# Kernel optimization log

Measured on AMD Instinct MI355X. Metric: run time of the kernel, lower is better.

## Reference

```python
import jax, jax.numpy as jnp
import numpy as np
import math

H = 16
D_MODEL = 1024
D_K = D_MODEL // H
MAX_REL = 32
B, S = 2, 2048


def setup_inputs() -> dict:
    key = jax.random.key(0)
    ks = jax.random.split(key, 12)
    def w(k):
        return jax.random.normal(k, (D_MODEL, D_MODEL), jnp.float32) * 0.02
    def b(k):
        return jax.random.normal(k, (D_MODEL,), jnp.float32) * 0.02
    return {
        "query": jax.random.normal(ks[0], (B, S, D_MODEL), jnp.float32),
        "key": jax.random.normal(ks[1], (B, S, D_MODEL), jnp.float32),
        "value": jax.random.normal(ks[2], (B, S, D_MODEL), jnp.float32),
        "mask": jax.random.randint(ks[3], (B, S, S), 0, 2, jnp.int32),
        "Wq": w(ks[4]), "bq": b(ks[5]),
        "Wk": w(ks[6]), "bk": b(ks[7]),
        "Wv": w(ks[8]), "bv": b(ks[9]),
        "Wo": w(ks[10]), "bo": b(ks[11]),
        "rel_emb": jax.random.normal(jax.random.fold_in(key, 99), (2 * MAX_REL + 1, D_K), jnp.float32) * 0.02,
    }


def _rel_bias(q_len, k_len, rel_emb):
    # relative positions clamped to [-MAX_REL, MAX_REL], shifted to [0, 2*MAX_REL]
    rel = jnp.arange(q_len)[:, None] - jnp.arange(k_len)[None, :]
    rel = jnp.clip(rel, -MAX_REL, MAX_REL) + MAX_REL
    # embedding lookup then sum over d_k (torch code: permute(2,0,1).sum(0))
    return rel_emb[rel].sum(-1)  # [q_len, k_len], shared across heads/batch


def reference(query, key, value, mask, Wq, bq, Wk, bk, Wv, bv, Wo, bo, rel_emb):
    nb, qlen, _ = query.shape
    klen = key.shape[1]
    def proj(x, W, b):  # torch Linear: x @ W.T + b -> [B, L, H, D_K] -> [B, H, L, D_K]
        return (x @ W.T + b).reshape(nb, -1, H, D_K).transpose(0, 2, 1, 3)
    q = proj(query, Wq, bq)
    k = proj(key, Wk, bk)
    v = proj(value, Wv, bv)
    scores = jnp.einsum('bhqd,bhkd->bhqk', q, k) / math.sqrt(D_K)
    scores = scores + _rel_bias(qlen, klen, rel_emb)[None, None]
    scores = jnp.where(mask[:, None] == 0, -1e9, scores)
    p = jax.nn.softmax(scores, axis=-1)
    out = jnp.einsum('bhqk,bhkd->bhqd', p, v)
    out = out.transpose(0, 2, 1, 3).reshape(nb, -1, H * D_K)
    return out @ Wo.T + bo
```

## Files before the change

### kernel.cpp

```cpp
#include <hip/hip_runtime.h>
#include <hip/hip_bf16.h>
#include <stdint.h>
#include <math.h>

typedef __bf16 bf16;
typedef __attribute__((ext_vector_type(8))) __bf16 bf16x8;
typedef __attribute__((ext_vector_type(4))) float f32x4;

#define MFMA(a, b, c) __builtin_amdgcn_mfma_f32_16x16x32_bf16(a, b, c, 0, 0, 0)

__device__ __forceinline__ bf16x8 cvt8(const float* p) {
  f32x4 a = *(const f32x4*)p;
  f32x4 b = *(const f32x4*)(p + 4);
  bf16x8 o;
  o[0] = (bf16)a[0]; o[1] = (bf16)a[1]; o[2] = (bf16)a[2]; o[3] = (bf16)a[3];
  o[4] = (bf16)b[0]; o[5] = (bf16)b[1]; o[6] = (bf16)b[2]; o[7] = (bf16)b[3];
  return o;
}

__global__ __launch_bounds__(256) void cvt_bf16(
    const float* __restrict__ s0, const float* __restrict__ s1, const float* __restrict__ s2,
    const float* __restrict__ s3, const float* __restrict__ s4, const float* __restrict__ s5,
    const float* __restrict__ s6,
    bf16* __restrict__ d0, bf16* __restrict__ d1, bf16* __restrict__ d2,
    bf16* __restrict__ d3, bf16* __restrict__ d4, bf16* __restrict__ d5,
    bf16* __restrict__ d6) {
  const float* s; bf16* d; int n8;
  switch (blockIdx.y) {
    case 0: s = s0; d = d0; n8 = 524288; break;
    case 1: s = s1; d = d1; n8 = 524288; break;
    case 2: s = s2; d = d2; n8 = 524288; break;
    case 3: s = s3; d = d3; n8 = 131072; break;
    case 4: s = s4; d = d4; n8 = 131072; break;
    case 5: s = s5; d = d5; n8 = 131072; break;
    default: s = s6; d = d6; n8 = 131072; break;
  }
  for (int i = blockIdx.x * 256 + threadIdx.x; i < n8; i += gridDim.x * 256)
    *(bf16x8*)&d[(size_t)i * 8] = cvt8(&s[(size_t)i * 8]);
}

__global__ __launch_bounds__(256) void pack_mask(const int* __restrict__ mask,
                                                 unsigned long long* __restrict__ pm,
                                                 int nwords) {
  const int lane = threadIdx.x & 63;
  const int wave = blockIdx.x * (blockDim.x >> 6) + (threadIdx.x >> 6);
  const int nwaves = gridDim.x * (blockDim.x >> 6);
  for (int w = wave; w < nwords; w += nwaves) {
    int m = mask[(size_t)w * 64 + lane];
    unsigned long long bits = __ballot(m != 0);
    if (lane == 0) pm[w] = bits;
  }
}

template <int OUT>
__global__ __launch_bounds__(256) void gemm_bt(const bf16* __restrict__ X,
                                               const bf16* __restrict__ W,
                                               const float* __restrict__ bias,
                                               void* __restrict__ out_) {
  __shared__ __align__(16) bf16 As[128 * 32];
  __shared__ __align__(16) bf16 Bs[64 * 32];
  const int tid = threadIdx.x, lane = tid & 63, w = tid >> 6;
  const int r16 = lane & 15, g4 = lane >> 4;
  const int m0 = blockIdx.x * 128, n0 = blockIdx.y * 64;

  f32x4 acc[4][2] = {};

  const int ra = tid >> 2;
  const int ca = (tid & 3) << 3;

  bf16x8 xa0 = *(const bf16x8*)&X[(size_t)(m0 + ra) * 1024 + ca];
  bf16x8 xa1 = *(const bf16x8*)&X[(size_t)(m0 + 64 + ra) * 1024 + ca];
  bf16x8 xb0 = *(const bf16x8*)&W[(size_t)(n0 + ra) * 1024 + ca];
  *(bf16x8*)&As[ra * 32 + ca] = xa0;
  *(bf16x8*)&As[(ra + 64) * 32 + ca] = xa1;
  *(bf16x8*)&Bs[ra * 32 + ca] = xb0;
  __syncthreads();

  const int wm = (w >> 1) << 6, wn = (w & 1) << 5;

  for (int k0 = 0; k0 < 1024; k0 += 32) {
    if (k0 + 32 < 1024) {
      xa0 = *(const bf16x8*)&X[(size_t)(m0 + ra) * 1024 + k0 + 32 + ca];
      xa1 = *(const bf16x8*)&X[(size_t)(m0 + 64 + ra) * 1024 + k0 + 32 + ca];
      xb0 = *(const bf16x8*)&W[(size_t)(n0 + ra) * 1024 + k0 + 32 + ca];
    }
    bf16x8 af[4], bfr[2];
#pragma unroll
    for (int i = 0; i < 4; i++)
      af[i] = *(const bf16x8*)&As[(wm + i * 16 + r16) * 32 + g4 * 8];
#pragma unroll
    for (int j = 0; j < 2; j++)
      bfr[j] = *(const bf16x8*)&Bs[(wn + j * 16 + r16) * 32 + g4 * 8];
#pragma unroll
    for (int i = 0; i < 4; i++)
#pragma unroll
      for (int j = 0; j < 2; j++)
        acc[i][j] = MFMA(af[i], bfr[j], acc[i][j]);
    __syncthreads();
    if (k0 + 32 < 1024) {
      *(bf16x8*)&As[ra * 32 + ca] = xa0;
      *(bf16x8*)&As[(ra + 64) * 32 + ca] = xa1;
      *(bf16x8*)&Bs[ra * 32 + ca] = xb0;
      __syncthreads();
    }
  }

#pragma unroll
  for (int j = 0; j < 2; j++) {
    const int col = n0 + wn + j * 16 + r16;
    const float bv = bias[col];
#pragma unroll
    for (int i = 0; i < 4; i++) {
      const int row0 = m0 + wm + i * 16 + g4 * 4;
#pragma unroll
      for (int r = 0; r < 4; r++) {
        float v = acc[i][j][r] + bv;
        const int row = row0 + r;
        if (OUT) {
          const int bb = row >> 11, s = row & 2047, h = col >> 6, d = col & 63;
          ((bf16*)out_)[((((size_t)bb * 16 + h) * 2048 + s) << 6) + d] = (bf16)v;
        } else {
          ((float*)out_)[(size_t)row * 1024 + col] = v;
        }
      }
    }
  }
}

__global__ __launch_bounds__(256) void attn_fwd(const bf16* __restrict__ Q,
                                                const bf16* __restrict__ Kb,
                                                const bf16* __restrict__ Vb,
                                                const unsigned long long* __restrict__ pm,
                                                const float* __restrict__ rel,
                                                bf16* __restrict__ ao) {
  constexpr int PAD = 72;
  __shared__ __align__(16) bf16 Ks[64 * PAD];
  __shared__ __align__(16) bf16 Vs[64 * 64];
  __shared__ __align__(16) bf16 Ps[64 * PAD];
  __shared__ float rb[65];

  const int tid = threadIdx.x, lane = tid & 63, w = tid >> 6;
  const int r16 = lane & 15, g4 = lane >> 4;
  const int qt = blockIdx.x;
  const int bh = blockIdx.y;
  const int b = bh >> 4, h = bh & 15;

  const bf16* Qh = Q + (size_t)bh * 2048 * 64;
  const bf16* Kh = Kb + (size_t)bh * 2048 * 64;
  const bf16* Vh = Vb + (size_t)bh * 2048 * 64;

  if (tid < 65) {
    const float* e = rel + tid * 64;
    float s = 0.f;
#pragma unroll
    for (int i = 0; i < 64; i++) s += e[i];
    rb[tid] = s;
  }

  bf16x8 aq[2];
  {
    const int qrow = (qt << 6) + (w << 4) + r16;
    aq[0] = *(const bf16x8*)&Qh[(size_t)qrow * 64 + g4 * 8];
    aq[1] = *(const bf16x8*)&Qh[(size_t)qrow * 64 + 32 + g4 * 8];
  }

  f32x4 acc_o[4] = {};
  float mreg[4] = {-1e30f, -1e30f, -1e30f, -1e30f};
  float lreg[4] = {0.f, 0.f, 0.f, 0.f};

  int skey[2], sf8[2], svcol[2];
#pragma unroll
  for (int cc = 0; cc < 2; cc++) {
    const int c = tid + (cc << 8);
    skey[cc] = c >> 3;
    sf8[cc] = (c & 7) << 3;
    svcol[cc] = (((skey[cc] >> 3) ^ (c & 7)) << 3) | (skey[cc] & 7);
  }

  bf16x8 kreg[2], vreg[2];
#pragma unroll
  for (int cc = 0; cc < 2; cc++) {
    kreg[cc] = *(const bf16x8*)&Kh[(size_t)skey[cc] * 64 + sf8[cc]];
    vreg[cc] = *(const bf16x8*)&Vh[(size_t)skey[cc] * 64 + sf8[cc]];
  }
#pragma unroll
  for (int cc = 0; cc < 2; cc++) {
    *(bf16x8*)&Ks[skey[cc] * PAD + sf8[cc]] = kreg[cc];
#pragma unroll
    for (int j = 0; j < 8; j++) Vs[((sf8[cc] + j) << 6) | svcol[cc]] = vreg[cc][j];
  }
  __syncthreads();

  for (int t = 0; t < 32; t++) {
    if (t < 31) {
#pragma unroll
      for (int cc = 0; cc < 2; cc++) {
        kreg[cc] = *(const bf16x8*)&Kh[(size_t)(((t + 1) << 6) + skey[cc]) * 64 + sf8[cc]];
        vreg[cc] = *(const bf16x8*)&Vh[(size_t)(((t + 1) << 6) + skey[cc]) * 64 + sf8[cc]];
      }
    }
    unsigned long long mw[4];
    const int qrow0 = (qt << 6) + (w << 4) + (g4 << 2);
#pragma unroll
    for (int r = 0; r < 4; r++)
      mw[r] = pm[(size_t)((b << 11) + qrow0 + r) * 32 + t];

    f32x4 sc[4];
#pragma unroll
    for (int f = 0; f < 4; f++) {
      f32x4 a = {};
#pragma unroll
      for (int kk = 0; kk < 2; kk++) {
        bf16x8 bk_ = *(const bf16x8*)&Ks[(f * 16 + r16) * PAD + kk * 32 + g4 * 8];
        a = MFMA(aq[kk], bk_, a);
      }
      sc[f] = a;
    }

    float s_[4][4];
#pragma unroll
    for (int f = 0; f < 4; f++) {
      const int kcol = (t << 6) + (f << 4) + r16;
#pragma unroll
      for (int r = 0; r < 4; r++) {
        int dd = (qrow0 + r) - kcol;
        dd = dd < -32 ? -32 : (dd > 32 ? 32 : dd);
        const bool on = (mw[r] >> ((f << 4) + r16)) & 1ull;
        s_[f][r] = on ? sc[f][r] * 0.125f + rb[dd + 32] : -1e9f;
      }
    }

    float rs[4];
#pragma unroll
    for (int r = 0; r < 4; r++) {
      float v = fmaxf(fmaxf(s_[0][r], s_[1][r]), fmaxf(s_[2][r], s_[3][r]));
#pragma unroll
      for (int d = 1; d < 16; d <<= 1) v = fmaxf(v, __shfl_xor(v, d, 16));
      const float mn = fmaxf(mreg[r], v);
      rs[r] = __expf(mreg[r] - mn);
      mreg[r] = mn;
    }
    float ps_[4] = {0.f, 0.f, 0.f, 0.f};
#pragma unroll
    for (int f = 0; f < 4; f++)
#pragma unroll
      for (int r = 0; r < 4; r++) {
        const float p = __expf(s_[f][r] - mreg[r]);
        ps_[r] += p;
        Ps[(w * 16 + g4 * 4 + r) * PAD + f * 16 + r16] = (bf16)p;
      }
#pragma unroll
    for (int r = 0; r < 4; r++) {
      float v = ps_[r];
#pragma unroll
      for (int d = 1; d < 16; d <<= 1) v += __shfl_xor(v, d, 16);
      lreg[r] = lreg[r] * rs[r] + v;
    }
#pragma unroll
    for (int f = 0; f < 4; f++)
#pragma unroll
      for (int r = 0; r < 4; r++) acc_o[f][r] *= rs[r];

#pragma unroll
    for (int kk = 0; kk < 2; kk++) {
      bf16x8 ap = *(const bf16x8*)&Ps[(w * 16 + r16) * PAD + kk * 32 + g4 * 8];
#pragma unroll
      for (int f = 0; f < 4; f++) {
        const int d = f * 16 + r16;
        bf16x8 bv_ = *(const bf16x8*)&Vs[(d << 6) | ((((kk << 2) + g4) ^ (d >> 3)) << 3)];
        acc_o[f] = MFMA(ap, bv_, acc_o[f]);
      }
    }
    __syncthreads();
    if (t < 31) {
#pragma unroll
      for (int cc = 0; cc < 2; cc++) {
        *(bf16x8*)&Ks[skey[cc] * PAD + sf8[cc]] = kreg[cc];
#pragma unroll
        for (int j = 0; j < 8; j++) Vs[((sf8[cc] + j) << 6) | svcol[cc]] = vreg[cc][j];
      }
      __syncthreads();
    }
  }

  const int qrow0 = (qt << 6) + (w << 4) + (g4 << 2);
#pragma unroll
  for (int r = 0; r < 4; r++) {
    const float inv = 1.f / lreg[r];
#pragma unroll
    for (int f = 0; f < 4; f++) {
      float v = acc_o[f][r] * inv;
      ao[(size_t)((b << 11) + qrow0 + r) * 1024 + (h << 6) + f * 16 + r16] = (bf16)v;
    }
  }
}

extern "C" void kernel_launch(void* const* d_in, const int* in_sizes, int n_in,
                              void* d_out, int out_size, void* d_ws, size_t ws_size,
                              hipStream_t stream) {
  const float* query = (const float*)d_in[0];
  const float* key   = (const float*)d_in[1];
  const float* value = (const float*)d_in[2];
  const int*   mask  = (const int*)d_in[3];
  const float* Wq = (const float*)d_in[4];
  const float* bq = (const float*)d_in[5];
  const float* Wk = (const float*)d_in[6];
  const float* bk = (const float*)d_in[7];
  const float* Wv = (const float*)d_in[8];
  const float* bv = (const float*)d_in[9];
  const float* Wo = (const float*)d_in[10];
  const float* bo = (const float*)d_in[11];
  const float* rel = (const float*)d_in[12];

  char* ws = (char*)d_ws;
  bf16* Qb = (bf16*)ws;
  bf16* Kb = (bf16*)(ws + 8388608);
  bf16* Vb = (bf16*)(ws + 16777216);
  bf16* AO = (bf16*)(ws + 25165824);
  unsigned long long* PM = (unsigned long long*)(ws + 33554432);
  bf16* qc  = (bf16*)(ws + 34603008);
  bf16* kc  = (bf16*)(ws + 42991616);
  bf16* vc  = (bf16*)(ws + 51380224);
  bf16* wqc = (bf16*)(ws + 59768832);
  bf16* wkc = (bf16*)(ws + 61865984);
  bf16* wvc = (bf16*)(ws + 63963136);
  bf16* woc = (bf16*)(ws + 66060288);

  cvt_bf16<<<dim3(256, 7), 256, 0, stream>>>(query, key, value, Wq, Wk, Wv, Wo,
                                             qc, kc, vc, wqc, wkc, wvc, woc);
  pack_mask<<<256, 256, 0, stream>>>(mask, PM, 2 * 2048 * 32);

  dim3 g(32, 16);
  gemm_bt<1><<<g, 256, 0, stream>>>(qc, wqc, bq, Qb);
  gemm_bt<1><<<g, 256, 0, stream>>>(kc, wkc, bk, Kb);
  gemm_bt<1><<<g, 256, 0, stream>>>(vc, wvc, bv, Vb);

  attn_fwd<<<dim3(32, 32), 256, 0, stream>>>(Qb, Kb, Vb, PM, rel, AO);

  gemm_bt<0><<<g, 256, 0, stream>>>(AO, woc, bo, (float*)d_out);
}
```

Baseline: 458.3 us.

## Enlarge GEMM tiles with direct global-to-LDS loads; exp2 softmax and swizzled P tile

The projection GEMM tile grows from 128x64 to 128x128 per block, and operands are loaded straight into LDS with global_load_lds instead of being staged through registers. The register prefetch that used to overlap the next tile's load with compute is gone, so every k-step now waits on a barrier after the load. In attention, log2(e) is folded into the score scale and relative bias so that exp2f replaces __expf. The padded P buffer becomes an XOR-swizzled 64x64 layout to avoid LDS bank conflicts and save shared memory.

```diff
diff --git a/kernel.cpp b/kernel.cpp
--- a/kernel.cpp
+++ b/kernel.cpp
@@ -8,6 +8,13 @@
 typedef __attribute__((ext_vector_type(4))) float f32x4;
 
 #define MFMA(a, b, c) __builtin_amdgcn_mfma_f32_16x16x32_bf16(a, b, c, 0, 0, 0)
+
+typedef __attribute__((address_space(3))) uint32_t lds_u32;
+typedef __attribute__((address_space(1))) const uint32_t glb_u32;
+
+__device__ __forceinline__ void gload16(const void* g, void* l) {
+  __builtin_amdgcn_global_load_lds((glb_u32*)g, (lds_u32*)l, 16, 0, 0);
+}
 
 __device__ __forceinline__ bf16x8 cvt8(const float* p) {
   f32x4 a = *(const f32x4*)p;
@@ -58,55 +65,40 @@
                                                const float* __restrict__ bias,
                                                void* __restrict__ out_) {
   __shared__ __align__(16) bf16 As[128 * 32];
-  __shared__ __align__(16) bf16 Bs[64 * 32];
+  __shared__ __align__(16) bf16 Bs[128 * 32];
   const int tid = threadIdx.x, lane = tid & 63, w = tid >> 6;
   const int r16 = lane & 15, g4 = lane >> 4;
-  const int m0 = blockIdx.x * 128, n0 = blockIdx.y * 64;
-
-  f32x4 acc[4][2] = {};
-
+  const int m0 = blockIdx.x * 128, n0 = blockIdx.y * 128;
+
+  f32x4 acc[4][4] = {};
   const int ra = tid >> 2;
   const int ca = (tid & 3) << 3;
-
-  bf16x8 xa0 = *(const bf16x8*)&X[(size_t)(m0 + ra) * 1024 + ca];
-  bf16x8 xa1 = *(const bf16x8*)&X[(size_t)(m0 + 64 + ra) * 1024 + ca];
-  bf16x8 xb0 = *(const bf16x8*)&W[(size_t)(n0 + ra) * 1024 + ca];
-  *(bf16x8*)&As[ra * 32 + ca] = xa0;
-  *(bf16x8*)&As[(ra + 64) * 32 + ca] = xa1;
-  *(bf16x8*)&Bs[ra * 32 + ca] = xb0;
-  __syncthreads();
-
-  const int wm = (w >> 1) << 6, wn = (w & 1) << 5;
+  const int wm = (w >> 1) << 6, wn = (w & 1) << 6;
 
   for (int k0 = 0; k0 < 1024; k0 += 32) {
-    if (k0 + 32 < 1024) {
-      xa0 = *(const bf16x8*)&X[(size_t)(m0 + ra) * 1024 + k0 + 32 + ca];
-      xa1 = *(const bf16x8*)&X[(size_t)(m0 + 64 + ra) * 1024 + k0 + 32 + ca];
-      xb0 = *(const bf16x8*)&W[(size_t)(n0 + ra) * 1024 + k0 + 32 + ca];
-    }
-    bf16x8 af[4], bfr[2];
+    gload16(&X[(size_t)(m0 + ra) * 1024 + k0 + ca],      &As[w << 9]);
+    gload16(&X[(size_t)(m0 + 64 + ra) * 1024 + k0 + ca], &As[2048 + (w << 9)]);
+    gload16(&W[(size_t)(n0 + ra) * 1024 + k0 + ca],      &Bs[w << 9]);
+    gload16(&W[(size_t)(n0 + 64 + ra) * 1024 + k0 + ca], &Bs[2048 + (w << 9)]);
+    __syncthreads();
+
+    bf16x8 af[4], bfr[4];
 #pragma unroll
     for (int i = 0; i < 4; i++)
       af[i] = *(const bf16x8*)&As[(wm + i * 16 + r16) * 32 + g4 * 8];
 #pragma unroll
-    for (int j = 0; j < 2; j++)
+    for (int j = 0; j < 4; j++)
       bfr[j] = *(const bf16x8*)&Bs[(wn + j * 16 + r16) * 32 + g4 * 8];
 #pragma unroll
     for (int i = 0; i < 4; i++)
 #pragma unroll
-      for (int j = 0; j < 2; j++)
+      for (int j = 0; j < 4; j++)
         acc[i][j] = MFMA(af[i], bfr[j], acc[i][j]);
     __syncthreads();
-    if (k0 + 32 < 1024) {
-      *(bf16x8*)&As[ra * 32 + ca] = xa0;
-      *(bf16x8*)&As[(ra + 64) * 32 + ca] = xa1;
-      *(bf16x8*)&Bs[ra * 32 + ca] = xb0;
-      __syncthreads();
-    }
-  }
-
-#pragma unroll
-  for (int j = 0; j < 2; j++) {
+  }
+
+#pragma unroll
+  for (int j = 0; j < 4; j++) {
     const int col = n0 + wn + j * 16 + r16;
     const float bv = bias[col];
 #pragma unroll
@@ -134,9 +126,10 @@
                                                 const float* __restrict__ rel,
                                                 bf16* __restrict__ ao) {
   constexpr int PAD = 72;
+  constexpr float SCL = 0.125f * 1.44269504f;
   __shared__ __align__(16) bf16 Ks[64 * PAD];
   __shared__ __align__(16) bf16 Vs[64 * 64];
-  __shared__ __align__(16) bf16 Ps[64 * PAD];
+  __shared__ __align__(16) bf16 Ps[64 * 64];
   __shared__ float rb[65];
 
   const int tid = threadIdx.x, lane = tid & 63, w = tid >> 6;
@@ -154,7 +147,7 @@
     float s = 0.f;
 #pragma unroll
     for (int i = 0; i < 64; i++) s += e[i];
-    rb[tid] = s;
+    rb[tid] = s * 1.44269504f;
   }
 
   bf16x8 aq[2];
@@ -226,7 +219,7 @@
         int dd = (qrow0 + r) - kcol;
         dd = dd < -32 ? -32 : (dd > 32 ? 32 : dd);
         const bool on = (mw[r] >> ((f << 4) + r16)) & 1ull;
-        s_[f][r] = on ? sc[f][r] * 0.125f + rb[dd + 32] : -1e9f;
+        s_[f][r] = on ? sc[f][r] * SCL + rb[dd + 32] : -1e9f;
       }
     }
 
@@ -237,17 +230,21 @@
 #pragma unroll
       for (int d = 1; d < 16; d <<= 1) v = fmaxf(v, __shfl_xor(v, d, 16));
       const float mn = fmaxf(mreg[r], v);
-      rs[r] = __expf(mreg[r] - mn);
+      rs[r] = exp2f(mreg[r] - mn);
       mreg[r] = mn;
     }
     float ps_[4] = {0.f, 0.f, 0.f, 0.f};
+    const int qsw = (g4 * 2) & 7;
 #pragma unroll
     for (int f = 0; f < 4; f++)
 #pragma unroll
       for (int r = 0; r < 4; r++) {
-        const float p = __expf(s_[f][r] - mreg[r]);
+        const float p = exp2f(s_[f][r] - mreg[r]);
         ps_[r] += p;
-        Ps[(w * 16 + g4 * 4 + r) * PAD + f * 16 + r16] = (bf16)p;
+        const int qr = (w << 4) + (g4 << 2) + r;
+        const int g = (f << 1) | (r16 >> 3);
+        const int gs = g ^ ((qsw + (r >> 1)) & 7);
+        Ps[(qr << 6) | (gs << 3) | (r16 & 7)] = (bf16)p;
       }
 #pragma unroll
     for (int r = 0; r < 4; r++) {
@@ -263,7 +260,8 @@
 
 #pragma unroll
     for (int kk = 0; kk < 2; kk++) {
-      bf16x8 ap = *(const bf16x8*)&Ps[(w * 16 + r16) * PAD + kk * 32 + g4 * 8];
+      const int pgs = ((kk << 2) | g4) ^ ((r16 >> 1) & 7);
+      bf16x8 ap = *(const bf16x8*)&Ps[(((w << 4) | r16) << 6) | (pgs << 3)];
 #pragma unroll
       for (int f = 0; f < 4; f++) {
         const int d = f * 16 + r16;
@@ -330,7 +328,7 @@
                                              qc, kc, vc, wqc, wkc, wvc, woc);
   pack_mask<<<256, 256, 0, stream>>>(mask, PM, 2 * 2048 * 32);
 
-  dim3 g(32, 16);
+  dim3 g(32, 8);
   gemm_bt<1><<<g, 256, 0, stream>>>(qc, wqc, bq, Qb);
   gemm_bt<1><<<g, 256, 0, stream>>>(kc, wkc, bk, Kb);
   gemm_bt<1><<<g, 256, 0, stream>>>(vc, wvc, bv, Vb);
```

After: 501.2 us. +9.4%, slower.
